# Optimization experiments

Measured on AMD Instinct MI355X. Metric: run time of the kernel, lower is better.

The kernel has to match this reference:

```python
import jax, jax.numpy as jnp
import numpy as np
import math

WS = 8          # window_size
H = 16          # num_heads
C = 512         # dim
D = C // H      # head dim


def _relative_coords_table():
    # (2*WS-1, 2*WS-1, 2), Swin-V2 log-spaced continuous coords
    r = jnp.arange(-(WS - 1), WS, dtype=jnp.float32)
    t = jnp.stack(jnp.meshgrid(r, r, indexing='ij'), axis=-1)
    t = t / (WS - 1) * 8.0
    return jnp.sign(t) * jnp.log2(jnp.abs(t) + 1.0) / np.float32(np.log2(8.0))


def _relative_position_index():
    # (WS*WS, WS*WS) int32 indices into the (2*WS-1)^2 bias table
    coords = np.stack(np.meshgrid(np.arange(WS), np.arange(WS), indexing='ij'))  # (2,WS,WS)
    cf = coords.reshape(2, -1)                                # (2, N)
    rel = cf[:, :, None] - cf[:, None, :]                     # (2, N, N)
    rel = rel.transpose(1, 2, 0)                              # (N, N, 2)
    rel[:, :, 0] += WS - 1
    rel[:, :, 1] += WS - 1
    rel[:, :, 0] *= 2 * WS - 1
    return jnp.asarray(rel.sum(-1), dtype=jnp.int32)


def setup_inputs() -> dict:
    key = jax.random.key(0)
    ks = jax.random.split(key, 9)
    B, N = 2048, WS * WS
    s = 0.02
    return {
        'hidden_states': jax.random.normal(ks[0], (B, N, C), jnp.float32),
        'q_w': jax.random.normal(ks[1], (C, C), jnp.float32) * s,
        'q_b': jnp.zeros((C,), jnp.float32),
        'k_w': jax.random.normal(ks[2], (C, C), jnp.float32) * s,
        'v_w': jax.random.normal(ks[3], (C, C), jnp.float32) * s,
        'v_b': jnp.zeros((C,), jnp.float32),
        'logit_scale': jnp.full((H, 1, 1), np.float32(math.log(10.0))),
        'cpb_w1': jax.random.normal(ks[4], (512, 2), jnp.float32) * s,
        'cpb_b1': jnp.zeros((512,), jnp.float32),
        'cpb_w2': jax.random.normal(ks[5], (H, 512), jnp.float32) * s,
    }


def reference(hidden_states, q_w, q_b, k_w, v_w, v_b, logit_scale,
              cpb_w1, cpb_b1, cpb_w2):
    B, N, _ = hidden_states.shape

    def heads(x):  # (B,N,C) -> (B,H,N,D)
        return x.reshape(B, N, H, D).transpose(0, 2, 1, 3)

    q = heads(hidden_states @ q_w.T + q_b)
    k = heads(hidden_states @ k_w.T)
    v = heads(hidden_states @ v_w.T + v_b)

    # cosine-similarity attention with clamped learnable logit scale
    qn = q / jnp.linalg.norm(q, axis=-1, keepdims=True)
    kn = k / jnp.linalg.norm(k, axis=-1, keepdims=True)
    scale = jnp.exp(jnp.minimum(logit_scale, np.float32(math.log(100.0))))  # (H,1,1)
    scores = jnp.einsum('bhnd,bhmd->bhnm', qn, kn) * scale

    # continuous relative position bias MLP + gather + sigmoid scale
    table = _relative_coords_table().reshape(-1, 2)            # (225, 2)
    hbias = jax.nn.relu(table @ cpb_w1.T + cpb_b1) @ cpb_w2.T  # (225, H)
    idx = _relative_position_index().reshape(-1)               # (N*N,)
    rpb = hbias[idx].reshape(N, N, H).transpose(2, 0, 1)       # (H, N, N)
    scores = scores + 16.0 * jax.nn.sigmoid(rpb)[None]

    probs = jax.nn.softmax(scores, axis=-1)
    ctx = jnp.einsum('bhnm,bhmd->bhnd', probs, v)
    return ctx.transpose(0, 2, 1, 3).reshape(B, N, C)
```

## Files before the change

kernel.cpp:

```cpp
#include <hip/hip_runtime.h>
#include <hip/hip_bf16.h>
#include <cstdint>
#include <cstddef>

typedef __attribute__((ext_vector_type(4))) float f32x4;
typedef __attribute__((ext_vector_type(8))) short short8;
typedef unsigned short ushort_t;

__device__ __forceinline__ ushort_t f2bf(float f) {
  return __builtin_bit_cast(ushort_t, __float2bfloat16(f));
}
__device__ __forceinline__ void load_lds16(const void* g, void* l) {
  __builtin_amdgcn_global_load_lds((const __attribute__((address_space(1))) void*)g,
                                   (__attribute__((address_space(3))) void*)l, 16, 0, 0);
}

#define LOG2E 1.4426950408889634f

__device__ __forceinline__ int swzA(int row, int b) { return row*128 + (b ^ ((row & 7) << 4)); }
__device__ __forceinline__ int swzQ(int row, int b) { return row*64  + (b ^ (((row >> 1) & 3) << 4)); }
__device__ __forceinline__ int swzV(int d,   int b) { return d*256   + (b ^ ((d & 7) << 4)); }

__global__ __launch_bounds__(256) void k_cvt_bf16(const float4* __restrict__ in,
                                                  ushort_t* __restrict__ outp, int n4) {
  int i = blockIdx.x * 256 + threadIdx.x;
  int stride = gridDim.x * 256;
  for (; i < n4; i += stride) {
    float4 v = in[i];
    ushort4 o = { f2bf(v.x), f2bf(v.y), f2bf(v.z), f2bf(v.w) };
    *(ushort4*)(outp + (size_t)i * 4) = o;
  }
}

__global__ __launch_bounds__(256) void k_wcat(const float* __restrict__ qw, const float* __restrict__ qb,
                                              const float* __restrict__ kw, const float* __restrict__ vw,
                                              const float* __restrict__ vb,
                                              ushort_t* __restrict__ Wcat, float* __restrict__ bcat) {
  int o = blockIdx.x;
  int h = o / 96, r = o % 96;
  const float* src; float bias;
  if (r < 32)      { src = qw + (size_t)(h*32 + r)      * 512; bias = qb[h*32 + r]; }
  else if (r < 64) { src = kw + (size_t)(h*32 + r - 32) * 512; bias = 0.f; }
  else             { src = vw + (size_t)(h*32 + r - 64) * 512; bias = vb[h*32 + r - 64]; }
  int t = threadIdx.x;
  Wcat[(size_t)o*512 + t]       = f2bf(src[t]);
  Wcat[(size_t)o*512 + t + 256] = f2bf(src[t + 256]);
  if (t == 0) bcat[o] = bias;
}

__global__ __launch_bounds__(256) void k_bias(const float* __restrict__ w1, const float* __restrict__ b1,
                                              const float* __restrict__ w2, float* __restrict__ bias16) {
  int t = blockIdx.x;
  int a = t / 15, b = t % 15;
  float x = (float)(a - 7) * (8.f / 7.f);
  float y = (float)(b - 7) * (8.f / 7.f);
  float fx = (x == 0.f) ? 0.f : copysignf(log2f(fabsf(x) + 1.f) * (1.f / 3.f), x);
  float fy = (y == 0.f) ? 0.f : copysignf(log2f(fabsf(y) + 1.f) * (1.f / 3.f), y);
  int wv = threadIdx.x >> 6, lane = threadIdx.x & 63;
  float acc[4] = {0.f, 0.f, 0.f, 0.f};
  for (int it = 0; it < 8; ++it) {
    int j = it*64 + lane;
    float act = fmaxf(fx * w1[2*j] + fy * w1[2*j + 1] + b1[j], 0.f);
#pragma unroll
    for (int hh = 0; hh < 4; ++hh)
      acc[hh] += act * w2[(wv*4 + hh)*512 + j];
  }
#pragma unroll
  for (int hh = 0; hh < 4; ++hh) {
    float v = acc[hh];
    for (int s = 1; s < 64; s <<= 1) v += __shfl_xor(v, s);
    if (lane == 0) bias16[t*16 + wv*4 + hh] = LOG2E * 16.f / (1.f + __expf(-v));
  }
}

#define BBASE 24576
#define KS_OFF 8192
#define VT_OFF 16384
#define PS_OFF 24576

__global__ __launch_bounds__(256) void k_main(const ushort_t* __restrict__ hbf,
                                              const ushort_t* __restrict__ Wcat,
                                              const float* __restrict__ bcat,
                                              const float* __restrict__ bias16,
                                              const float* __restrict__ lscale,
                                              float* __restrict__ out) {
  __shared__ __align__(128) char lb_raw[43008];
  char* lb = lb_raw;

  int bid = blockIdx.x;
  int wg = (bid & 7) * 2048 + (bid >> 3);
  int mtile = wg >> 4;
  int h     = wg & 15;

  int tid = threadIdx.x;
  int w = tid >> 6, lane = tid & 63;
  int lm = lane & 15, lg = lane >> 4;

  const ushort_t* Ag = hbf  + (size_t)mtile * 128 * 512;
  const ushort_t* Wg = Wcat + (size_t)h * 96 * 512;

  int rA0 = w*32      + (lane >> 2);
  int rA1 = w*32 + 16 + (lane >> 2);
  int rB0 = w*16      + (lane >> 2);
  int rB1 = 64 + w*16 + (lane >> 2);
  int sl  = lane & 3;
  int offA0 = rA0*512 + (sl ^ ((rA0 >> 1) & 3))*8;
  int offA1 = rA1*512 + (sl ^ ((rA1 >> 1) & 3))*8;
  int offB0 = rB0*512 + (sl ^ ((rB0 >> 1) & 3))*8;
  int offB1 = rB1*512 + (sl ^ ((rB1 >> 1) & 3))*8;

  f32x4 acc[2][6] = {};

#define STAGE(ksn, bsel) do {                                                  \
    int kk0 = (ksn) * 32;                                                      \
    load_lds16(Ag + offA0 + kk0, lb + (bsel)*8192 + (w*2+0)*1024);             \
    load_lds16(Ag + offA1 + kk0, lb + (bsel)*8192 + (w*2+1)*1024);             \
    load_lds16(Wg + offB0 + kk0, lb + BBASE + (bsel)*6144 + w*1024);           \
    if (w < 2)                                                                 \
      load_lds16(Wg + offB1 + kk0, lb + BBASE + (bsel)*6144 + (4+w)*1024);     \
  } while (0)

  STAGE(0, 0);
#pragma unroll
  for (int ks = 0; ks < 16; ++ks) {
    int cur = ks % 3;
    if (ks < 15) {
      STAGE(ks + 1, (ks + 1) % 3);
      if (w < 2) asm volatile("s_waitcnt vmcnt(4)" ::: "memory");
      else       asm volatile("s_waitcnt vmcnt(3)" ::: "memory");
    } else {
      asm volatile("s_waitcnt vmcnt(0)" ::: "memory");
    }
    asm volatile("s_barrier" ::: "memory");

    const char* Ab = lb + cur*8192;
    const char* Bb = lb + BBASE + cur*6144;
    short8 av0 = *(const short8*)(Ab + swzQ(w*32      + lm, lg*16));
    short8 av1 = *(const short8*)(Ab + swzQ(w*32 + 16 + lm, lg*16));
    short8 bv[6];
#pragma unroll
    for (int j = 0; j < 6; ++j)
      bv[j] = *(const short8*)(Bb + swzQ(j*16 + lm, lg*16));
#pragma unroll
    for (int j = 0; j < 6; ++j)
      acc[0][j] = __builtin_amdgcn_mfma_f32_16x16x32_bf16(av0, bv[j], acc[0][j], 0, 0, 0);
#pragma unroll
    for (int j = 0; j < 6; ++j)
      acc[1][j] = __builtin_amdgcn_mfma_f32_16x16x32_bf16(av1, bv[j], acc[1][j], 0, 0, 0);
  }
#undef STAGE
  asm volatile("s_barrier" ::: "memory");

  float scl = __expf(fminf(lscale[h], 4.6051701860f)) * LOG2E;
  float bb[6];
#pragma unroll
  for (int nj = 0; nj < 6; ++nj) bb[nj] = bcat[h*96 + nj*16 + lm];

#pragma unroll
  for (int i = 0; i < 2; ++i) {
#pragma unroll
    for (int r = 0; r < 4; ++r) {
      float q0 = acc[i][0][r] + bb[0], q1 = acc[i][1][r] + bb[1];
      float k0 = acc[i][2][r],         k1 = acc[i][3][r];
      float ssq = q0*q0 + q1*q1;
      float ssk = k0*k0 + k1*k1;
      ssq += __shfl_xor(ssq, 1); ssq += __shfl_xor(ssq, 2);
      ssq += __shfl_xor(ssq, 4); ssq += __shfl_xor(ssq, 8);
      ssk += __shfl_xor(ssk, 1); ssk += __shfl_xor(ssk, 2);
      ssk += __shfl_xor(ssk, 4); ssk += __shfl_xor(ssk, 8);
      float rq = rsqrtf(ssq) * scl;
      float rk = rsqrtf(ssk);
      int row = w*32 + i*16 + lg*4 + r;
      *(ushort_t*)(lb + swzQ(row, lm*2))                  = f2bf(q0 * rq);
      *(ushort_t*)(lb + swzQ(row, 32 + lm*2))             = f2bf(q1 * rq);
      *(ushort_t*)(lb + KS_OFF + swzQ(row, lm*2))         = f2bf(k0 * rk);
      *(ushort_t*)(lb + KS_OFF + swzQ(row, 32 + lm*2))    = f2bf(k1 * rk);
    }
#pragma unroll
    for (int j = 0; j < 2; ++j) {
      ushort4 pk;
      pk.x = f2bf(acc[i][4+j][0] + bb[4+j]);
      pk.y = f2bf(acc[i][4+j][1] + bb[4+j]);
      pk.z = f2bf(acc[i][4+j][2] + bb[4+j]);
      pk.w = f2bf(acc[i][4+j][3] + bb[4+j]);
      int d = j*16 + lm, tokb = (w*32 + i*16 + lg*4) * 2;
      *(ushort4*)(lb + VT_OFF + swzV(d, tokb)) = pk;
    }
  }
  __syncthreads();

  float bfrag[4][4];
#pragma unroll
  for (int ci = 0; ci < 4; ++ci) {
    int m = ci*16 + lm, rm = m >> 3, cm = m & 7;
#pragma unroll
    for (int r = 0; r < 4; ++r) {
      int n = w*16 + lg*4 + r;
      int idx = ((n >> 3) - rm + 7)*15 + ((n & 7) - cm + 7);
      bfrag[ci][r] = bias16[idx*16 + h];
    }
  }

#pragma unroll
  for (int win = 0; win < 2; ++win) {
    short8 aq = *(const short8*)(lb + swzQ(win*64 + w*16 + lm, lg*16));
    f32x4 p[4];
#pragma unroll
    for (int ci = 0; ci < 4; ++ci) {
      short8 bk = *(const short8*)(lb + KS_OFF + swzQ(win*64 + ci*16 + lm, lg*16));
      f32x4 z = {0.f, 0.f, 0.f, 0.f};
      f32x4 s = __builtin_amdgcn_mfma_f32_16x16x32_bf16(aq, bk, z, 0, 0, 0);
#pragma unroll
      for (int r = 0; r < 4; ++r)
        p[ci][r] = __builtin_amdgcn_exp2f(s[r] + bfrag[ci][r]);
    }
#pragma unroll
    for (int ci = 0; ci < 4; ++ci)
#pragma unroll
      for (int r = 0; r < 4; ++r) {
        int row = w*16 + lg*4 + r;
        *(ushort_t*)(lb + PS_OFF + swzA(row, (ci*16 + lm)*2)) = f2bf(p[ci][r]);
      }
    float rs[4];
#pragma unroll
    for (int r = 0; r < 4; ++r) {
      float s = p[0][r] + p[1][r] + p[2][r] + p[3][r];
      s += __shfl_xor(s, 1); s += __shfl_xor(s, 2);
      s += __shfl_xor(s, 4); s += __shfl_xor(s, 8);
      rs[r] = 1.f / s;
    }
    f32x4 oacc[2] = {};
#pragma unroll
    for (int kk = 0; kk < 2; ++kk) {
      short8 ap = *(const short8*)(lb + PS_OFF + swzA(w*16 + lm, kk*64 + lg*16));
#pragma unroll
      for (int ci = 0; ci < 2; ++ci) {
        short8 bvv = *(const short8*)(lb + VT_OFF + swzV(ci*16 + lm, win*128 + kk*64 + lg*16));
        oacc[ci] = __builtin_amdgcn_mfma_f32_16x16x32_bf16(ap, bvv, oacc[ci], 0, 0, 0);
      }
    }
    size_t gw = (size_t)mtile*2 + win;
#pragma unroll
    for (int ci = 0; ci < 2; ++ci)
#pragma unroll
      for (int r = 0; r < 4; ++r) {
        int n = w*16 + lg*4 + r;
        out[(gw*64 + n)*512 + h*32 + ci*16 + lm] = oacc[ci][r] * rs[r];
      }
  }
}

extern "C" void kernel_launch(void* const* d_in, const int* in_sizes, int n_in,
                              void* d_out, int out_size, void* d_ws, size_t ws_size,
                              hipStream_t stream) {
  (void)in_sizes; (void)n_in; (void)out_size; (void)ws_size;
  const float* hidden = (const float*)d_in[0];
  const float* q_w    = (const float*)d_in[1];
  const float* q_b    = (const float*)d_in[2];
  const float* k_w    = (const float*)d_in[3];
  const float* v_w    = (const float*)d_in[4];
  const float* v_b    = (const float*)d_in[5];
  const float* lscale = (const float*)d_in[6];
  const float* cpb_w1 = (const float*)d_in[7];
  const float* cpb_b1 = (const float*)d_in[8];
  const float* cpb_w2 = (const float*)d_in[9];
  float* out = (float*)d_out;

  char* wsb = (char*)d_ws;
  ushort_t* hbf    = (ushort_t*)wsb;
  ushort_t* Wcat   = (ushort_t*)(wsb + 134217728);
  float*    bcat   = (float*)(wsb + 135790592);
  float*    bias16 = (float*)(wsb + 135796736);

  hipLaunchKernelGGL(k_cvt_bf16, dim3(2048), dim3(256), 0, stream,
                     (const float4*)hidden, hbf, 16777216);
  hipLaunchKernelGGL(k_wcat, dim3(1536), dim3(256), 0, stream,
                     q_w, q_b, k_w, v_w, v_b, Wcat, bcat);
  hipLaunchKernelGGL(k_bias, dim3(225), dim3(256), 0, stream,
                     cpb_w1, cpb_b1, cpb_w2, bias16);
  hipLaunchKernelGGL(k_main, dim3(16384), dim3(256), 0, stream,
                     hbf, Wcat, bcat, bias16, lscale, out);
}
```

Before: 468.1 us.

## Load weight fragments directly into registers instead of staging through LDS

The weight (B) tiles for the fused QKV projection are now loaded straight from global memory into register fragments, prefetched one k-step ahead, rather than staged through shared memory. This shrinks LDS use from 43 KB to 32 KB and adds a launch-bounds occupancy hint of 4 blocks. Hand-tuned vmcnt waits and sched barriers order the register prefetch against the A-tile async LDS copies. In exchange each wave issues its own uncoalesced-ish global loads for W, with no reuse across waves, which raises L2 traffic and register pressure.

```diff
diff --git a/kernel.cpp b/kernel.cpp
--- a/kernel.cpp
+++ b/kernel.cpp
@@ -14,6 +14,8 @@
   __builtin_amdgcn_global_load_lds((const __attribute__((address_space(1))) void*)g,
                                    (__attribute__((address_space(3))) void*)l, 16, 0, 0);
 }
+#define FENCE() do { asm volatile("" ::: "memory"); \
+                     __builtin_amdgcn_sched_barrier(0); } while (0)
 
 #define LOG2E 1.4426950408889634f
 
@@ -73,18 +75,17 @@
   }
 }
 
-#define BBASE 24576
 #define KS_OFF 8192
 #define VT_OFF 16384
 #define PS_OFF 24576
 
-__global__ __launch_bounds__(256) void k_main(const ushort_t* __restrict__ hbf,
-                                              const ushort_t* __restrict__ Wcat,
-                                              const float* __restrict__ bcat,
-                                              const float* __restrict__ bias16,
-                                              const float* __restrict__ lscale,
-                                              float* __restrict__ out) {
-  __shared__ __align__(128) char lb_raw[43008];
+__global__ __launch_bounds__(256, 4) void k_main(const ushort_t* __restrict__ hbf,
+                                                 const ushort_t* __restrict__ Wcat,
+                                                 const float* __restrict__ bcat,
+                                                 const float* __restrict__ bias16,
+                                                 const float* __restrict__ lscale,
+                                                 float* __restrict__ out) {
+  __shared__ __align__(128) char lb_raw[32768];
   char* lb = lb_raw;
 
   int bid = blockIdx.x;
@@ -101,54 +102,61 @@
 
   int rA0 = w*32      + (lane >> 2);
   int rA1 = w*32 + 16 + (lane >> 2);
-  int rB0 = w*16      + (lane >> 2);
-  int rB1 = 64 + w*16 + (lane >> 2);
   int sl  = lane & 3;
   int offA0 = rA0*512 + (sl ^ ((rA0 >> 1) & 3))*8;
   int offA1 = rA1*512 + (sl ^ ((rA1 >> 1) & 3))*8;
-  int offB0 = rB0*512 + (sl ^ ((rB0 >> 1) & 3))*8;
-  int offB1 = rB1*512 + (sl ^ ((rB1 >> 1) & 3))*8;
+
+  const ushort_t* Bg = Wg + lm*512 + lg*8;
 
   f32x4 acc[2][6] = {};
-
-#define STAGE(ksn, bsel) do {                                                  \
+  short8 bv[6];
+
+#define STAGE_A(ksn, bsel) do {                                                \
     int kk0 = (ksn) * 32;                                                      \
     load_lds16(Ag + offA0 + kk0, lb + (bsel)*8192 + (w*2+0)*1024);             \
     load_lds16(Ag + offA1 + kk0, lb + (bsel)*8192 + (w*2+1)*1024);             \
-    load_lds16(Wg + offB0 + kk0, lb + BBASE + (bsel)*6144 + w*1024);           \
-    if (w < 2)                                                                 \
-      load_lds16(Wg + offB1 + kk0, lb + BBASE + (bsel)*6144 + (4+w)*1024);     \
   } while (0)
 
-  STAGE(0, 0);
+  STAGE_A(0, 0);
+  FENCE();
+#pragma unroll
+  for (int j = 0; j < 6; ++j)
+    bv[j] = *(const short8*)(Bg + j*8192);
+  FENCE();
+
 #pragma unroll
   for (int ks = 0; ks < 16; ++ks) {
     int cur = ks % 3;
     if (ks < 15) {
-      STAGE(ks + 1, (ks + 1) % 3);
-      if (w < 2) asm volatile("s_waitcnt vmcnt(4)" ::: "memory");
-      else       asm volatile("s_waitcnt vmcnt(3)" ::: "memory");
+      STAGE_A(ks + 1, (ks + 1) % 3);
+      asm volatile("s_waitcnt vmcnt(8)" ::: "memory");
     } else {
-      asm volatile("s_waitcnt vmcnt(0)" ::: "memory");
+      asm volatile("s_waitcnt vmcnt(6)" ::: "memory");
     }
     asm volatile("s_barrier" ::: "memory");
 
     const char* Ab = lb + cur*8192;
-    const char* Bb = lb + BBASE + cur*6144;
     short8 av0 = *(const short8*)(Ab + swzQ(w*32      + lm, lg*16));
     short8 av1 = *(const short8*)(Ab + swzQ(w*32 + 16 + lm, lg*16));
-    short8 bv[6];
-#pragma unroll
-    for (int j = 0; j < 6; ++j)
-      bv[j] = *(const short8*)(Bb + swzQ(j*16 + lm, lg*16));
+    if (ks < 15) asm volatile("s_waitcnt vmcnt(2)" ::: "memory");
+    else         asm volatile("s_waitcnt vmcnt(0)" ::: "memory");
+
 #pragma unroll
     for (int j = 0; j < 6; ++j)
       acc[0][j] = __builtin_amdgcn_mfma_f32_16x16x32_bf16(av0, bv[j], acc[0][j], 0, 0, 0);
 #pragma unroll
     for (int j = 0; j < 6; ++j)
       acc[1][j] = __builtin_amdgcn_mfma_f32_16x16x32_bf16(av1, bv[j], acc[1][j], 0, 0, 0);
-  }
-#undef STAGE
+
+    if (ks < 15) {
+      FENCE();
+#pragma unroll
+      for (int j = 0; j < 6; ++j)
+        bv[j] = *(const short8*)(Bg + j*8192 + (ks + 1)*32);
+      FENCE();
+    }
+  }
+#undef STAGE_A
   asm volatile("s_barrier" ::: "memory");
 
   float scl = __expf(fminf(lscale[h], 4.6051701860f)) * LOG2E;
```

After: 890.7 us. 1.9x slower.
